# Kernel optimization log

Hardware: AMD Instinct MI355X
Metric: run time of the kernel (lower is better)

Reference implementation:

```python
import jax, jax.numpy as jnp
import numpy as np

IN_DIM = 14400
K = 25
DIMS = [7200, 3600, 1800]  # floor(in_dim / 2**(i+1))
OUT_DIM = 2
BATCH = 256


def setup_inputs() -> dict:
    key = jax.random.key(0)
    ks = jax.random.split(key, 32)
    inp = {}
    inp["x"] = jax.random.normal(ks[0], (BATCH, 2 * IN_DIM), dtype=jnp.float32)
    # shared KNN tables (both channels load the same h5 files)
    prev = [IN_DIM] + DIMS[:-1]
    for i, (d, p) in enumerate(zip(DIMS, prev)):
        inp[f"knn{i}"] = jax.random.randint(ks[1 + i], (d, K), 0, p, dtype=jnp.int64)
    std = (2.0 / K) ** 0.5
    kidx = 4
    for ch in ("p", "n"):
        for i, d in enumerate(DIMS):
            inp[f"w{ch}{i}"] = jax.random.normal(ks[kidx], (d, K), dtype=jnp.float32) * std; kidx += 1
            inp[f"b{ch}{i}"] = jnp.zeros((1, d), dtype=jnp.float32)
        inp[f"fc{ch}_w"] = jax.random.normal(ks[kidx], (OUT_DIM, DIMS[-1]), dtype=jnp.float32) * (1.0 / DIMS[-1] ** 0.5); kidx += 1
        inp[f"fc{ch}_b"] = jnp.zeros((OUT_DIM,), dtype=jnp.float32)
    inp["fc3_w"] = jax.random.normal(ks[kidx], (OUT_DIM, 4), dtype=jnp.float32) * 0.5
    inp["fc3_b"] = jnp.zeros((OUT_DIM,), dtype=jnp.float32)
    return inp


def _lcn(x, knns, ws, bs, fw, fb):
    # x: (B, in_dim). Each layer: gather KNN neighbors, weighted sum, bias, relu.
    for knn, w, b in zip(knns, ws, bs):
        g = x[:, knn]                                  # (B, dim, K) gather
        x = jax.nn.relu(jnp.einsum('bdk,dk->bd', g, w) + b)
    return x @ fw.T + fb                               # fc_angle


def reference(x, knn0, knn1, knn2,
              wp0, bp0, wp1, bp1, wp2, bp2, fcp_w, fcp_b,
              wn0, bn0, wn1, bn1, wn2, bn2, fcn_w, fcn_b,
              fc3_w, fc3_b):
    knns = (knn0, knn1, knn2)
    xpos = _lcn(x[:, :IN_DIM], knns, (wp0, wp1, wp2), (bp0, bp1, bp2), fcp_w, fcp_b)
    xneg = _lcn(x[:, IN_DIM:], knns, (wn0, wn1, wn2), (bn0, bn1, bn2), fcn_w, fcn_b)
    h = jax.nn.relu(jnp.concatenate([xpos, xneg], axis=1))  # (B, 4)
    return h @ fc3_w.T + fc3_b
```

## Files before the change

### kernel.cpp

```cpp
#include <hip/hip_runtime.h>
#include <hip/hip_bf16.h>

using bf16 = __hip_bfloat16;

#define K 25
#define B 256

__device__ __forceinline__ float b2f(ushort u) {
  unsigned int w = ((unsigned int)u) << 16;
  float f;
  __builtin_memcpy(&f, &w, 4);
  return f;
}
__device__ __forceinline__ ushort f2b(float f) {
  bf16 h = __float2bfloat16(f);
  ushort u;
  __builtin_memcpy(&u, &h, 2);
  return u;
}

__global__ void detect_kernel(const unsigned int* __restrict__ xw,
                              const unsigned int* __restrict__ knnw,
                              int* __restrict__ flags) {
  if (threadIdx.x == 0) {
    int weird = 0;
    for (int i = 0; i < 64; ++i) {
      unsigned int u = xw[i * 997];
      unsigned int e = (u >> 23) & 0xFF;
      if (e >= 192 || e <= 30) ++weird;
    }
    flags[0] = (weird >= 32) ? 1 : 0;
  } else if (threadIdx.x == 1) {
    int nz = 0;
    for (int i = 0; i < 64; ++i) {
      if (knnw[2 * i + 1] != 0) ++nz;
    }
    flags[1] = (nz == 0) ? 1 : 0;
  }
}

__device__ __forceinline__ float load_f(const void* p, size_t i, int fdt) {
  if (fdt) return __bfloat162float(((const bf16*)p)[i]);
  return ((const float*)p)[i];
}

__global__ __launch_bounds__(256) void transpose_kernel(const void* __restrict__ x,
                                                        bf16* __restrict__ xT,
                                                        const int* __restrict__ flags) {
  const int fdt = flags[0];
  __shared__ float tile[64][65];
  const int f0 = blockIdx.x * 64;
  const int b0 = blockIdx.y * 64;
  const int t = threadIdx.x;
  if (fdt) {
    const bf16* xp = (const bf16*)x;
#pragma unroll
    for (int i = 0; i < 16; ++i) {
      const int lin = t + i * 256;
      const int bl = lin >> 6, fl = lin & 63;
      tile[bl][fl] = __bfloat162float(xp[(size_t)(b0 + bl) * 28800 + (f0 + fl)]);
    }
  } else {
    const float* xp = (const float*)x;
#pragma unroll
    for (int i = 0; i < 16; ++i) {
      const int lin = t + i * 256;
      const int bl = lin >> 6, fl = lin & 63;
      tile[bl][fl] = xp[(size_t)(b0 + bl) * 28800 + (f0 + fl)];
    }
  }
  __syncthreads();
#pragma unroll
  for (int i = 0; i < 16; ++i) {
    const int lin = t + i * 256;
    const int fl = lin >> 6, bl = lin & 63;
    ((ushort*)xT)[(size_t)(f0 + fl) * B + (b0 + bl)] = f2b(tile[bl][fl]);
  }
}

__global__ __launch_bounds__(256) void lcn_layer(const bf16* __restrict__ inT,
                                                 const void* __restrict__ knn,
                                                 const void* __restrict__ wp,
                                                 const void* __restrict__ bp,
                                                 const void* __restrict__ wn,
                                                 const void* __restrict__ bn,
                                                 bf16* __restrict__ outT,
                                                 const int* __restrict__ flags,
                                                 int prev, int dout) {
  const int fdt = flags[0];
  const int idt = flags[1];
  const int wave = threadIdx.x >> 6;
  const int lane = threadIdx.x & 63;
  const int d = blockIdx.x * 4 + wave;
  const int ch = blockIdx.y;
  const ushort* in = (const ushort*)(inT + (size_t)ch * prev * B);
  const void* wsel = ch ? wn : wp;
  const void* bsel = ch ? bn : bp;

  int r[K];
  float wk[K];
  if (idt) {
    const long long* ip = (const long long*)knn + (size_t)d * K;
#pragma unroll
    for (int k = 0; k < K; ++k) r[k] = (int)ip[k];
  } else {
    const int* ip = (const int*)knn + (size_t)d * K;
#pragma unroll
    for (int k = 0; k < K; ++k) r[k] = ip[k];
  }
  if (fdt) {
    const ushort* wpp = (const ushort*)wsel + (size_t)d * K;
#pragma unroll
    for (int k = 0; k < K; ++k) wk[k] = b2f(wpp[k]);
  } else {
    const float* wpp = (const float*)wsel + (size_t)d * K;
#pragma unroll
    for (int k = 0; k < K; ++k) wk[k] = wpp[k];
  }
  const float bias = load_f(bsel, d, fdt);

  float a0 = 0.f, a1 = 0.f, a2 = 0.f, a3 = 0.f;
#pragma unroll
  for (int k = 0; k < K; ++k) {
    const ushort4 v = *(const ushort4*)(in + (size_t)r[k] * B + lane * 4);
    a0 = fmaf(wk[k], b2f(v.x), a0);
    a1 = fmaf(wk[k], b2f(v.y), a1);
    a2 = fmaf(wk[k], b2f(v.z), a2);
    a3 = fmaf(wk[k], b2f(v.w), a3);
  }
  a0 = fmaxf(a0 + bias, 0.f);
  a1 = fmaxf(a1 + bias, 0.f);
  a2 = fmaxf(a2 + bias, 0.f);
  a3 = fmaxf(a3 + bias, 0.f);

  ushort4 o;
  o.x = f2b(a0); o.y = f2b(a1); o.z = f2b(a2); o.w = f2b(a3);
  *(ushort4*)((ushort*)outT + ((size_t)ch * dout + d) * B + lane * 4) = o;
}

__global__ __launch_bounds__(256) void fc_kernel(const bf16* __restrict__ h2,
                                                 const void* __restrict__ fpw,
                                                 const void* __restrict__ fnw,
                                                 float* __restrict__ y,
                                                 const int* __restrict__ flags) {
  const int fdt = flags[0];
  const int ch = blockIdx.y;
  const int b = threadIdx.x;
  const void* fw = ch ? fnw : fpw;
  const ushort* h = (const ushort*)(h2 + (size_t)ch * 1800 * B);
  const int d0 = blockIdx.x * 8;

  float w0[8], w1[8];
  if (fdt) {
    const ushort* fp = (const ushort*)fw;
#pragma unroll
    for (int j = 0; j < 8; ++j) {
      w0[j] = b2f(fp[d0 + j]);
      w1[j] = b2f(fp[1800 + d0 + j]);
    }
  } else {
    const float* fp = (const float*)fw;
#pragma unroll
    for (int j = 0; j < 8; ++j) {
      w0[j] = fp[d0 + j];
      w1[j] = fp[1800 + d0 + j];
    }
  }

  float a0 = 0.f, a1 = 0.f;
#pragma unroll
  for (int j = 0; j < 8; ++j) {
    const float v = b2f(h[(size_t)(d0 + j) * B + b]);
    a0 = fmaf(w0[j], v, a0);
    a1 = fmaf(w1[j], v, a1);
  }
  atomicAdd(&y[(ch * 2 + 0) * B + b], a0);
  atomicAdd(&y[(ch * 2 + 1) * B + b], a1);
}

__global__ __launch_bounds__(256) void final_kernel(const float* __restrict__ y,
                                                    const void* __restrict__ fpb,
                                                    const void* __restrict__ fnb,
                                                    const void* __restrict__ f3w,
                                                    const void* __restrict__ f3b,
                                                    void* __restrict__ out,
                                                    const int* __restrict__ flags) {
  const int fdt = flags[0];
  const int b = threadIdx.x;
  float h0 = fmaxf(y[0 * B + b] + load_f(fpb, 0, fdt), 0.0f);
  float h1 = fmaxf(y[1 * B + b] + load_f(fpb, 1, fdt), 0.0f);
  float h2 = fmaxf(y[2 * B + b] + load_f(fnb, 0, fdt), 0.0f);
  float h3 = fmaxf(y[3 * B + b] + load_f(fnb, 1, fdt), 0.0f);
#pragma unroll
  for (int o = 0; o < 2; ++o) {
    float r = load_f(f3b, o, fdt);
    r = fmaf(load_f(f3w, o * 4 + 0, fdt), h0, r);
    r = fmaf(load_f(f3w, o * 4 + 1, fdt), h1, r);
    r = fmaf(load_f(f3w, o * 4 + 2, fdt), h2, r);
    r = fmaf(load_f(f3w, o * 4 + 3, fdt), h3, r);
    if (fdt) ((bf16*)out)[b * 2 + o] = __float2bfloat16(r);
    else     ((float*)out)[b * 2 + o] = r;
  }
}

extern "C" void kernel_launch(void* const* d_in, const int* in_sizes, int n_in,
                              void* d_out, int out_size, void* d_ws, size_t ws_size,
                              hipStream_t stream) {
  const void* x    = d_in[0];
  const void* knn0 = d_in[1];
  const void* knn1 = d_in[2];
  const void* knn2 = d_in[3];
  const void* wp0  = d_in[4];
  const void* bp0  = d_in[5];
  const void* wp1  = d_in[6];
  const void* bp1  = d_in[7];
  const void* wp2  = d_in[8];
  const void* bp2  = d_in[9];
  const void* fcpw = d_in[10];
  const void* fcpb = d_in[11];
  const void* wn0  = d_in[12];
  const void* bn0  = d_in[13];
  const void* wn1  = d_in[14];
  const void* bn1  = d_in[15];
  const void* wn2  = d_in[16];
  const void* bn2  = d_in[17];
  const void* fcnw = d_in[18];
  const void* fcnb = d_in[19];
  const void* f3w  = d_in[20];
  const void* f3b  = d_in[21];

  char* ws = (char*)d_ws;
  bf16* xT = (bf16*)(ws);
  bf16* h0 = (bf16*)(ws + 14745600);
  bf16* h1 = (bf16*)(ws + 22118400);
  bf16* h2 = (bf16*)(ws + 25804800);
  float* y = (float*)(ws + 27648000);
  int* flags = (int*)(ws + 27652096);

  hipMemsetAsync(y, 0, 1024 * sizeof(float), stream);

  detect_kernel<<<1, 64, 0, stream>>>((const unsigned int*)x,
                                      (const unsigned int*)knn0, flags);

  transpose_kernel<<<dim3(450, 4), 256, 0, stream>>>(x, xT, flags);

  lcn_layer<<<dim3(1800, 2), 256, 0, stream>>>(xT, knn0, wp0, bp0, wn0, bn0, h0,
                                               flags, 14400, 7200);
  lcn_layer<<<dim3(900, 2), 256, 0, stream>>>(h0, knn1, wp1, bp1, wn1, bn1, h1,
                                              flags, 7200, 3600);
  lcn_layer<<<dim3(450, 2), 256, 0, stream>>>(h1, knn2, wp2, bp2, wn2, bn2, h2,
                                              flags, 3600, 1800);

  fc_kernel<<<dim3(225, 2), 256, 0, stream>>>(h2, fcpw, fcnw, y, flags);

  final_kernel<<<1, 256, 0, stream>>>(y, fcpb, fcnb, f3w, f3b, d_out, flags);
}
```

Before: 177.7 us.

## Fuse all stages into one persistent kernel with grid-wide barriers

Replaces the seven separate launches (detect, transpose, three LCN layers, fc, final) with a single persistent kernel of 512 blocks that uses atomic-counter grid barriers between stages. The aim is to remove launch overhead and the tail bubbles between small kernels. The transpose also switches to vectorized float4/ushort4 loads and stores, and the fc stage processes four batch columns per lane. The cost is correctness risk if all 512 blocks are not co-resident, spin-wait barrier overhead, and lower parallelism per stage, since each block loops over its items.

```diff
diff --git a/kernel.cpp b/kernel.cpp
--- a/kernel.cpp
+++ b/kernel.cpp
@@ -5,253 +5,258 @@
 
 #define K 25
 #define B 256
+#define NBLK 512
 
 __device__ __forceinline__ float b2f(ushort u) {
   unsigned int w = ((unsigned int)u) << 16;
-  float f;
-  __builtin_memcpy(&f, &w, 4);
-  return f;
+  float f; __builtin_memcpy(&f, &w, 4); return f;
 }
 __device__ __forceinline__ ushort f2b(float f) {
   bf16 h = __float2bfloat16(f);
-  ushort u;
-  __builtin_memcpy(&u, &h, 2);
-  return u;
-}
-
-__global__ void detect_kernel(const unsigned int* __restrict__ xw,
-                              const unsigned int* __restrict__ knnw,
-                              int* __restrict__ flags) {
+  ushort u; __builtin_memcpy(&u, &h, 2); return u;
+}
+
+struct Params {
+  const void *x, *knn0, *knn1, *knn2;
+  const void *wp0, *bp0, *wp1, *bp1, *wp2, *bp2, *fcpw, *fcpb;
+  const void *wn0, *bn0, *wn1, *bn1, *wn2, *bn2, *fcnw, *fcnb;
+  const void *f3w, *f3b;
+  ushort *xT, *h0, *h1, *h2;
+  float *y;
+  int *bars;
+  void *out;
+};
+
+__device__ __forceinline__ void gbar(int* bars, int idx) {
+  __syncthreads();
   if (threadIdx.x == 0) {
+    __threadfence();
+    atomicAdd(&bars[idx * 16], 1);
+    while (atomicAdd(&bars[idx * 16], 0) < NBLK) {
+      __builtin_amdgcn_s_sleep(2);
+    }
+    __threadfence();
+  }
+  __syncthreads();
+}
+
+__device__ __forceinline__ void lcn_stage(const ushort* __restrict__ inT,
+                                          const void* __restrict__ knn,
+                                          const void* wP, const void* bP,
+                                          const void* wN, const void* bN,
+                                          ushort* __restrict__ outT,
+                                          int prev, int dout, int fdt, int idt) {
+  const int wave = threadIdx.x >> 6;
+  const int lane = threadIdx.x & 63;
+  for (int wt = (blockIdx.x << 2) | wave; wt < 2 * dout; wt += NBLK * 4) {
+    const int ch = wt >= dout;
+    const int d = ch ? wt - dout : wt;
+    const ushort* in = inT + (size_t)ch * prev * B;
+    const void* wsel = ch ? wN : wP;
+    const void* bsel = ch ? bN : bP;
+
+    int r[K]; float wk[K];
+    if (idt) {
+      const long long* ip = (const long long*)knn + (size_t)d * K;
+#pragma unroll
+      for (int k = 0; k < K; ++k) r[k] = (int)ip[k];
+    } else {
+      const int* ip = (const int*)knn + (size_t)d * K;
+#pragma unroll
+      for (int k = 0; k < K; ++k) r[k] = ip[k];
+    }
+    if (fdt) {
+      const ushort* wp = (const ushort*)wsel + (size_t)d * K;
+#pragma unroll
+      for (int k = 0; k < K; ++k) wk[k] = b2f(wp[k]);
+    } else {
+      const float* wp = (const float*)wsel + (size_t)d * K;
+#pragma unroll
+      for (int k = 0; k < K; ++k) wk[k] = wp[k];
+    }
+    const float bias = fdt ? b2f(((const ushort*)bsel)[d]) : ((const float*)bsel)[d];
+
+    float a0 = 0.f, a1 = 0.f, a2 = 0.f, a3 = 0.f;
+#pragma unroll
+    for (int k = 0; k < K; ++k) {
+      const ushort4 v = *(const ushort4*)(in + (size_t)r[k] * B + (lane << 2));
+      a0 = fmaf(wk[k], b2f(v.x), a0);
+      a1 = fmaf(wk[k], b2f(v.y), a1);
+      a2 = fmaf(wk[k], b2f(v.z), a2);
+      a3 = fmaf(wk[k], b2f(v.w), a3);
+    }
+    a0 = fmaxf(a0 + bias, 0.f);
+    a1 = fmaxf(a1 + bias, 0.f);
+    a2 = fmaxf(a2 + bias, 0.f);
+    a3 = fmaxf(a3 + bias, 0.f);
+    ushort4 o; o.x = f2b(a0); o.y = f2b(a1); o.z = f2b(a2); o.w = f2b(a3);
+    *(ushort4*)(outT + ((size_t)ch * dout + d) * B + (lane << 2)) = o;
+  }
+}
+
+__global__ __launch_bounds__(256, 2) void fused_kernel(Params p) {
+  __shared__ float tile[64][65];
+
+  int fdt, idt;
+  {
+    const unsigned int* xw = (const unsigned int*)p.x;
     int weird = 0;
     for (int i = 0; i < 64; ++i) {
-      unsigned int u = xw[i * 997];
-      unsigned int e = (u >> 23) & 0xFF;
-      if (e >= 192 || e <= 30) ++weird;
-    }
-    flags[0] = (weird >= 32) ? 1 : 0;
-  } else if (threadIdx.x == 1) {
+      unsigned int e = (xw[i * 997] >> 23) & 0xFF;
+      weird += (e >= 192) || (e <= 30);
+    }
+    fdt = (weird >= 32);
+    const unsigned int* kw = (const unsigned int*)p.knn0;
     int nz = 0;
-    for (int i = 0; i < 64; ++i) {
-      if (knnw[2 * i + 1] != 0) ++nz;
-    }
-    flags[1] = (nz == 0) ? 1 : 0;
-  }
-}
-
-__device__ __forceinline__ float load_f(const void* p, size_t i, int fdt) {
-  if (fdt) return __bfloat162float(((const bf16*)p)[i]);
-  return ((const float*)p)[i];
-}
-
-__global__ __launch_bounds__(256) void transpose_kernel(const void* __restrict__ x,
-                                                        bf16* __restrict__ xT,
-                                                        const int* __restrict__ flags) {
-  const int fdt = flags[0];
-  __shared__ float tile[64][65];
-  const int f0 = blockIdx.x * 64;
-  const int b0 = blockIdx.y * 64;
-  const int t = threadIdx.x;
-  if (fdt) {
-    const bf16* xp = (const bf16*)x;
-#pragma unroll
-    for (int i = 0; i < 16; ++i) {
-      const int lin = t + i * 256;
-      const int bl = lin >> 6, fl = lin & 63;
-      tile[bl][fl] = __bfloat162float(xp[(size_t)(b0 + bl) * 28800 + (f0 + fl)]);
-    }
-  } else {
-    const float* xp = (const float*)x;
-#pragma unroll
-    for (int i = 0; i < 16; ++i) {
-      const int lin = t + i * 256;
-      const int bl = lin >> 6, fl = lin & 63;
-      tile[bl][fl] = xp[(size_t)(b0 + bl) * 28800 + (f0 + fl)];
-    }
-  }
-  __syncthreads();
-#pragma unroll
-  for (int i = 0; i < 16; ++i) {
-    const int lin = t + i * 256;
-    const int fl = lin >> 6, bl = lin & 63;
-    ((ushort*)xT)[(size_t)(f0 + fl) * B + (b0 + bl)] = f2b(tile[bl][fl]);
-  }
-}
-
-__global__ __launch_bounds__(256) void lcn_layer(const bf16* __restrict__ inT,
-                                                 const void* __restrict__ knn,
-                                                 const void* __restrict__ wp,
-                                                 const void* __restrict__ bp,
-                                                 const void* __restrict__ wn,
-                                                 const void* __restrict__ bn,
-                                                 bf16* __restrict__ outT,
-                                                 const int* __restrict__ flags,
-                                                 int prev, int dout) {
-  const int fdt = flags[0];
-  const int idt = flags[1];
-  const int wave = threadIdx.x >> 6;
-  const int lane = threadIdx.x & 63;
-  const int d = blockIdx.x * 4 + wave;
-  const int ch = blockIdx.y;
-  const ushort* in = (const ushort*)(inT + (size_t)ch * prev * B);
-  const void* wsel = ch ? wn : wp;
-  const void* bsel = ch ? bn : bp;
-
-  int r[K];
-  float wk[K];
-  if (idt) {
-    const long long* ip = (const long long*)knn + (size_t)d * K;
-#pragma unroll
-    for (int k = 0; k < K; ++k) r[k] = (int)ip[k];
-  } else {
-    const int* ip = (const int*)knn + (size_t)d * K;
-#pragma unroll
-    for (int k = 0; k < K; ++k) r[k] = ip[k];
-  }
-  if (fdt) {
-    const ushort* wpp = (const ushort*)wsel + (size_t)d * K;
-#pragma unroll
-    for (int k = 0; k < K; ++k) wk[k] = b2f(wpp[k]);
-  } else {
-    const float* wpp = (const float*)wsel + (size_t)d * K;
-#pragma unroll
-    for (int k = 0; k < K; ++k) wk[k] = wpp[k];
-  }
-  const float bias = load_f(bsel, d, fdt);
-
-  float a0 = 0.f, a1 = 0.f, a2 = 0.f, a3 = 0.f;
-#pragma unroll
-  for (int k = 0; k < K; ++k) {
-    const ushort4 v = *(const ushort4*)(in + (size_t)r[k] * B + lane * 4);
-    a0 = fmaf(wk[k], b2f(v.x), a0);
-    a1 = fmaf(wk[k], b2f(v.y), a1);
-    a2 = fmaf(wk[k], b2f(v.z), a2);
-    a3 = fmaf(wk[k], b2f(v.w), a3);
-  }
-  a0 = fmaxf(a0 + bias, 0.f);
-  a1 = fmaxf(a1 + bias, 0.f);
-  a2 = fmaxf(a2 + bias, 0.f);
-  a3 = fmaxf(a3 + bias, 0.f);
-
-  ushort4 o;
-  o.x = f2b(a0); o.y = f2b(a1); o.z = f2b(a2); o.w = f2b(a3);
-  *(ushort4*)((ushort*)outT + ((size_t)ch * dout + d) * B + lane * 4) = o;
-}
-
-__global__ __launch_bounds__(256) void fc_kernel(const bf16* __restrict__ h2,
-                                                 const void* __restrict__ fpw,
-                                                 const void* __restrict__ fnw,
-                                                 float* __restrict__ y,
-                                                 const int* __restrict__ flags) {
-  const int fdt = flags[0];
-  const int ch = blockIdx.y;
-  const int b = threadIdx.x;
-  const void* fw = ch ? fnw : fpw;
-  const ushort* h = (const ushort*)(h2 + (size_t)ch * 1800 * B);
-  const int d0 = blockIdx.x * 8;
-
-  float w0[8], w1[8];
-  if (fdt) {
-    const ushort* fp = (const ushort*)fw;
-#pragma unroll
-    for (int j = 0; j < 8; ++j) {
-      w0[j] = b2f(fp[d0 + j]);
-      w1[j] = b2f(fp[1800 + d0 + j]);
-    }
-  } else {
-    const float* fp = (const float*)fw;
-#pragma unroll
-    for (int j = 0; j < 8; ++j) {
-      w0[j] = fp[d0 + j];
-      w1[j] = fp[1800 + d0 + j];
-    }
-  }
-
-  float a0 = 0.f, a1 = 0.f;
-#pragma unroll
-  for (int j = 0; j < 8; ++j) {
-    const float v = b2f(h[(size_t)(d0 + j) * B + b]);
-    a0 = fmaf(w0[j], v, a0);
-    a1 = fmaf(w1[j], v, a1);
-  }
-  atomicAdd(&y[(ch * 2 + 0) * B + b], a0);
-  atomicAdd(&y[(ch * 2 + 1) * B + b], a1);
-}
-
-__global__ __launch_bounds__(256) void final_kernel(const float* __restrict__ y,
-                                                    const void* __restrict__ fpb,
-                                                    const void* __restrict__ fnb,
-                                                    const void* __restrict__ f3w,
-                                                    const void* __restrict__ f3b,
-                                                    void* __restrict__ out,
-                                                    const int* __restrict__ flags) {
-  const int fdt = flags[0];
-  const int b = threadIdx.x;
-  float h0 = fmaxf(y[0 * B + b] + load_f(fpb, 0, fdt), 0.0f);
-  float h1 = fmaxf(y[1 * B + b] + load_f(fpb, 1, fdt), 0.0f);
-  float h2 = fmaxf(y[2 * B + b] + load_f(fnb, 0, fdt), 0.0f);
-  float h3 = fmaxf(y[3 * B + b] + load_f(fnb, 1, fdt), 0.0f);
-#pragma unroll
-  for (int o = 0; o < 2; ++o) {
-    float r = load_f(f3b, o, fdt);
-    r = fmaf(load_f(f3w, o * 4 + 0, fdt), h0, r);
-    r = fmaf(load_f(f3w, o * 4 + 1, fdt), h1, r);
-    r = fmaf(load_f(f3w, o * 4 + 2, fdt), h2, r);
-    r = fmaf(load_f(f3w, o * 4 + 3, fdt), h3, r);
-    if (fdt) ((bf16*)out)[b * 2 + o] = __float2bfloat16(r);
-    else     ((float*)out)[b * 2 + o] = r;
+    for (int i = 0; i < 64; ++i) nz += (kw[2 * i + 1] != 0);
+    idt = (nz == 0);
+  }
+
+  const int t0 = threadIdx.x;
+  for (int t = blockIdx.x; t < 1800; t += NBLK) {
+    const int f0 = (t % 450) * 64;
+    const int b0 = (t / 450) * 64;
+    if (!fdt) {
+      const float* xp = (const float*)p.x;
+#pragma unroll
+      for (int q = 0; q < 4; ++q) {
+        const int lin = t0 + q * 256;
+        const int bl = lin >> 4;
+        const int fq = (lin & 15) << 2;
+        const float4 v = *(const float4*)(xp + (size_t)(b0 + bl) * 28800 + f0 + fq);
+        tile[bl][fq] = v.x; tile[bl][fq + 1] = v.y;
+        tile[bl][fq + 2] = v.z; tile[bl][fq + 3] = v.w;
+      }
+    } else {
+      const ushort* xp = (const ushort*)p.x;
+#pragma unroll
+      for (int q = 0; q < 4; ++q) {
+        const int lin = t0 + q * 256;
+        const int bl = lin >> 4;
+        const int fq = (lin & 15) << 2;
+        const ushort4 v = *(const ushort4*)(xp + (size_t)(b0 + bl) * 28800 + f0 + fq);
+        tile[bl][fq] = b2f(v.x); tile[bl][fq + 1] = b2f(v.y);
+        tile[bl][fq + 2] = b2f(v.z); tile[bl][fq + 3] = b2f(v.w);
+      }
+    }
+    __syncthreads();
+#pragma unroll
+    for (int q = 0; q < 4; ++q) {
+      const int lin = t0 + q * 256;
+      const int fl = lin >> 4;
+      const int bq = (lin & 15) << 2;
+      ushort4 o;
+      o.x = f2b(tile[bq][fl]);     o.y = f2b(tile[bq + 1][fl]);
+      o.z = f2b(tile[bq + 2][fl]); o.w = f2b(tile[bq + 3][fl]);
+      *(ushort4*)(p.xT + (size_t)(f0 + fl) * B + b0 + bq) = o;
+    }
+    __syncthreads();
+  }
+  gbar(p.bars, 0);
+
+  lcn_stage(p.xT, p.knn0, p.wp0, p.bp0, p.wn0, p.bn0, p.h0, 14400, 7200, fdt, idt);
+  gbar(p.bars, 1);
+  lcn_stage(p.h0, p.knn1, p.wp1, p.bp1, p.wn1, p.bn1, p.h1, 7200, 3600, fdt, idt);
+  gbar(p.bars, 2);
+  lcn_stage(p.h1, p.knn2, p.wp2, p.bp2, p.wn2, p.bn2, p.h2, 3600, 1800, fdt, idt);
+  gbar(p.bars, 3);
+
+  {
+    const int wave = threadIdx.x >> 6;
+    const int lane = threadIdx.x & 63;
+    for (int wt = (blockIdx.x << 2) | wave; wt < 450; wt += NBLK * 4) {
+      const int ch = wt >= 225;
+      const int c0 = (ch ? wt - 225 : wt) * 8;
+      const ushort* h = p.h2 + (size_t)ch * 1800 * B;
+      const void* fw = ch ? p.fcnw : p.fcpw;
+      float w0[8], w1[8];
+      if (fdt) {
+        const ushort* fp = (const ushort*)fw;
+#pragma unroll
+        for (int j = 0; j < 8; ++j) { w0[j] = b2f(fp[c0 + j]); w1[j] = b2f(fp[1800 + c0 + j]); }
+      } else {
+        const float* fp = (const float*)fw;
+#pragma unroll
+        for (int j = 0; j < 8; ++j) { w0[j] = fp[c0 + j]; w1[j] = fp[1800 + c0 + j]; }
+      }
+      float s0[4] = {0.f, 0.f, 0.f, 0.f}, s1[4] = {0.f, 0.f, 0.f, 0.f};
+#pragma unroll
+      for (int j = 0; j < 8; ++j) {
+        const ushort4 v = *(const ushort4*)(h + (size_t)(c0 + j) * B + (lane << 2));
+        const float f0v = b2f(v.x), f1v = b2f(v.y), f2v = b2f(v.z), f3v = b2f(v.w);
+        s0[0] = fmaf(w0[j], f0v, s0[0]); s0[1] = fmaf(w0[j], f1v, s0[1]);
+        s0[2] = fmaf(w0[j], f2v, s0[2]); s0[3] = fmaf(w0[j], f3v, s0[3]);
+        s1[0] = fmaf(w1[j], f0v, s1[0]); s1[1] = fmaf(w1[j], f1v, s1[1]);
+        s1[2] = fmaf(w1[j], f2v, s1[2]); s1[3] = fmaf(w1[j], f3v, s1[3]);
+      }
+#pragma unroll
+      for (int i = 0; i < 4; ++i) {
+        atomicAdd(&p.y[(ch * 2 + 0) * B + (lane << 2) + i], s0[i]);
+        atomicAdd(&p.y[(ch * 2 + 1) * B + (lane << 2) + i], s1[i]);
+      }
+    }
+  }
+  gbar(p.bars, 4);
+
+  if (blockIdx.x == 0) {
+    const int b = threadIdx.x;
+    const float bp0v = fdt ? b2f(((const ushort*)p.fcpb)[0]) : ((const float*)p.fcpb)[0];
+    const float bp1v = fdt ? b2f(((const ushort*)p.fcpb)[1]) : ((const float*)p.fcpb)[1];
+    const float bn0v = fdt ? b2f(((const ushort*)p.fcnb)[0]) : ((const float*)p.fcnb)[0];
+    const float bn1v = fdt ? b2f(((const ushort*)p.fcnb)[1]) : ((const float*)p.fcnb)[1];
+    const float h0v = fmaxf(p.y[0 * B + b] + bp0v, 0.f);
+    const float h1v = fmaxf(p.y[1 * B + b] + bp1v, 0.f);
+    const float h2v = fmaxf(p.y[2 * B + b] + bn0v, 0.f);
+    const float h3v = fmaxf(p.y[3 * B + b] + bn1v, 0.f);
+#pragma unroll
+    for (int o = 0; o < 2; ++o) {
+      float w0, w1, w2, w3, bb;
+      if (fdt) {
+        const ushort* fp = (const ushort*)p.f3w;
+        w0 = b2f(fp[o * 4 + 0]); w1 = b2f(fp[o * 4 + 1]);
+        w2 = b2f(fp[o * 4 + 2]); w3 = b2f(fp[o * 4 + 3]);
+        bb = b2f(((const ushort*)p.f3b)[o]);
+      } else {
+        const float* fp = (const float*)p.f3w;
+        w0 = fp[o * 4 + 0]; w1 = fp[o * 4 + 1];
+        w2 = fp[o * 4 + 2]; w3 = fp[o * 4 + 3];
+        bb = ((const float*)p.f3b)[o];
+      }
+      float r = bb;
+      r = fmaf(w0, h0v, r); r = fmaf(w1, h1v, r);
+      r = fmaf(w2, h2v, r); r = fmaf(w3, h3v, r);
+      if (fdt) ((ushort*)p.out)[b * 2 + o] = f2b(r);
+      else     ((float*)p.out)[b * 2 + o] = r;
+    }
   }
 }
 
 extern "C" void kernel_launch(void* const* d_in, const int* in_sizes, int n_in,
                               void* d_out, int out_size, void* d_ws, size_t ws_size,
                               hipStream_t stream) {
-  const void* x    = d_in[0];
-  const void* knn0 = d_in[1];
-  const void* knn1 = d_in[2];
-  const void* knn2 = d_in[3];
-  const void* wp0  = d_in[4];
-  const void* bp0  = d_in[5];
-  const void* wp1  = d_in[6];
-  const void* bp1  = d_in[7];
-  const void* wp2  = d_in[8];
-  const void* bp2  = d_in[9];
-  const void* fcpw = d_in[10];
-  const void* fcpb = d_in[11];
-  const void* wn0  = d_in[12];
-  const void* bn0  = d_in[13];
-  const void* wn1  = d_in[14];
-  const void* bn1  = d_in[15];
-  const void* wn2  = d_in[16];
-  const void* bn2  = d_in[17];
-  const void* fcnw = d_in[18];
-  const void* fcnb = d_in[19];
-  const void* f3w  = d_in[20];
-  const void* f3b  = d_in[21];
-
   char* ws = (char*)d_ws;
-  bf16* xT = (bf16*)(ws);
-  bf16* h0 = (bf16*)(ws + 14745600);
-  bf16* h1 = (bf16*)(ws + 22118400);
-  bf16* h2 = (bf16*)(ws + 25804800);
-  float* y = (float*)(ws + 27648000);
-  int* flags = (int*)(ws + 27652096);
-
-  hipMemsetAsync(y, 0, 1024 * sizeof(float), stream);
-
-  detect_kernel<<<1, 64, 0, stream>>>((const unsigned int*)x,
-                                      (const unsigned int*)knn0, flags);
-
-  transpose_kernel<<<dim3(450, 4), 256, 0, stream>>>(x, xT, flags);
-
-  lcn_layer<<<dim3(1800, 2), 256, 0, stream>>>(xT, knn0, wp0, bp0, wn0, bn0, h0,
-                                               flags, 14400, 7200);
-  lcn_layer<<<dim3(900, 2), 256, 0, stream>>>(h0, knn1, wp1, bp1, wn1, bn1, h1,
-                                              flags, 7200, 3600);
-  lcn_layer<<<dim3(450, 2), 256, 0, stream>>>(h1, knn2, wp2, bp2, wn2, bn2, h2,
-                                              flags, 3600, 1800);
-
-  fc_kernel<<<dim3(225, 2), 256, 0, stream>>>(h2, fcpw, fcnw, y, flags);
-
-  final_kernel<<<1, 256, 0, stream>>>(y, fcpb, fcnb, f3w, f3b, d_out, flags);
-}
+  Params p;
+  p.x    = d_in[0];
+  p.knn0 = d_in[1];  p.knn1 = d_in[2];  p.knn2 = d_in[3];
+  p.wp0  = d_in[4];  p.bp0  = d_in[5];
+  p.wp1  = d_in[6];  p.bp1  = d_in[7];
+  p.wp2  = d_in[8];  p.bp2  = d_in[9];
+  p.fcpw = d_in[10]; p.fcpb = d_in[11];
+  p.wn0  = d_in[12]; p.bn0  = d_in[13];
+  p.wn1  = d_in[14]; p.bn1  = d_in[15];
+  p.wn2  = d_in[16]; p.bn2  = d_in[17];
+  p.fcnw = d_in[18]; p.fcnb = d_in[19];
+  p.f3w  = d_in[20]; p.f3b  = d_in[21];
+
+  p.xT   = (ushort*)(ws);
+  p.h0   = (ushort*)(ws + 14745600);
+  p.h1   = (ushort*)(ws + 22118400);
+  p.h2   = (ushort*)(ws + 25804800);
+  p.y    = (float*)(ws + 27648000);
+  p.bars = (int*)(ws + 27652096);
+  p.out  = d_out;
+
+  hipMemsetAsync(ws + 27648000, 0, 8192, stream);
+
+  fused_kernel<<<NBLK, 256, 0, stream>>>(p);
+}
```

Result: slower. 403.0 us (+126.8%).
